# Optimization experiments

Measured on AMD Instinct MI355X. Metric: run time of the kernel, lower is better.

Reference implementation:

```python
import jax, jax.numpy as jnp
import numpy as np

N_NODES = 50000
N_EDGES = 800000
IN_CH, HID, OUT_CH, HEADS = 128, 32, 32, 8
NEG_SLOPE = 0.2


def setup_inputs() -> dict:
    key = jax.random.key(0)
    ks = jax.random.split(key, 20)
    x = jax.random.normal(ks[0], (N_NODES, IN_CH), dtype=jnp.float32)
    edge_index = jax.random.randint(ks[1], (2, N_EDGES), 0, N_NODES, dtype=jnp.int64)
    s = 0.1
    # encoder layer 1: in -> hid, heads=8 (concat)
    W1 = jax.random.normal(ks[2], (IN_CH, HEADS * HID), jnp.float32) * s
    as1 = jax.random.normal(ks[3], (HEADS, HID), jnp.float32) * s
    ad1 = jax.random.normal(ks[4], (HEADS, HID), jnp.float32) * s
    b1 = jnp.zeros((HEADS * HID,), jnp.float32)
    # encoder layer 2: hid*heads -> out, heads=1
    W2 = jax.random.normal(ks[5], (HEADS * HID, OUT_CH), jnp.float32) * s
    as2 = jax.random.normal(ks[6], (1, OUT_CH), jnp.float32) * s
    ad2 = jax.random.normal(ks[7], (1, OUT_CH), jnp.float32) * s
    b2 = jnp.zeros((OUT_CH,), jnp.float32)
    # decoder layer 1: out -> hid, heads=8 (concat)
    W3 = jax.random.normal(ks[8], (OUT_CH, HEADS * HID), jnp.float32) * s
    as3 = jax.random.normal(ks[9], (HEADS, HID), jnp.float32) * s
    ad3 = jax.random.normal(ks[10], (HEADS, HID), jnp.float32) * s
    b3 = jnp.zeros((HEADS * HID,), jnp.float32)
    # decoder layer 2: hid*heads -> in, heads=1
    W4 = jax.random.normal(ks[11], (HEADS * HID, IN_CH), jnp.float32) * s
    as4 = jax.random.normal(ks[12], (1, IN_CH), jnp.float32) * s
    ad4 = jax.random.normal(ks[13], (1, IN_CH), jnp.float32) * s
    b4 = jnp.zeros((IN_CH,), jnp.float32)
    return dict(x=x, edge_index=edge_index, W1=W1, as1=as1, ad1=ad1, b1=b1,
                W2=W2, as2=as2, ad2=ad2, b2=b2, W3=W3, as3=as3, ad3=ad3, b3=b3,
                W4=W4, as4=as4, ad4=ad4, b4=b4)


def gat_conv(x, src, dst, W, a_src, a_dst, b, heads, ch):
    # PyG GATConv: h = xW, e_ij = LeakyReLU(a_src.h_j + a_dst.h_i), softmax over incoming edges of i
    h = (x @ W).reshape(-1, heads, ch)                       # [N, H, C]
    al_s = jnp.sum(h * a_src[None], axis=-1)                 # [N, H]
    al_d = jnp.sum(h * a_dst[None], axis=-1)                 # [N, H]
    e = jax.nn.leaky_relu(al_s[src] + al_d[dst], NEG_SLOPE)  # [E, H]
    emax = jax.ops.segment_max(e, dst, num_segments=N_NODES)
    ee = jnp.exp(e - emax[dst])
    denom = jax.ops.segment_sum(ee, dst, num_segments=N_NODES)
    alpha = ee / denom[dst]                                  # [E, H]
    msg = alpha[:, :, None] * h[src]                         # [E, H, C]
    out = jax.ops.segment_sum(msg, dst, num_segments=N_NODES)  # [N, H, C]
    return out.reshape(N_NODES, heads * ch) + b


def reference(x, edge_index, W1, as1, ad1, b1, W2, as2, ad2, b2,
              W3, as3, ad3, b3, W4, as4, ad4, b4):
    # add self loops (PyG default add_self_loops=True)
    loop = jnp.arange(N_NODES, dtype=edge_index.dtype)
    src = jnp.concatenate([edge_index[0], loop])
    dst = jnp.concatenate([edge_index[1], loop])
    # encode
    z = gat_conv(x, src, dst, W1, as1, ad1, b1, HEADS, HID)
    z = jax.nn.relu(z)
    z = gat_conv(z, src, dst, W2, as2, ad2, b2, 1, OUT_CH)
    # decode
    r = gat_conv(z, src, dst, W3, as3, ad3, b3, HEADS, HID)
    r = jax.nn.relu(r)
    r = gat_conv(r, src, dst, W4, as4, ad4, b4, 1, IN_CH)
    return r
```

## Files before the change

kernel.cpp:

```cpp
#include <hip/hip_runtime.h>
#include <math.h>

#define N_NODES 50000
#define N_EDGES 800000
#define N_TOT   850000
#define NSB     ((N_NODES + 255) / 256)

typedef __attribute__((ext_vector_type(8))) short short8;
typedef __attribute__((ext_vector_type(4))) float floatx4;

__device__ __forceinline__ unsigned int pack_bf16x2(float a, float b) {
    unsigned ua = __float_as_uint(a);
    unsigned ub = __float_as_uint(b);
    ua += 0x7fff + ((ua >> 16) & 1);
    ub += 0x7fff + ((ub >> 16) & 1);
    return (ua >> 16) | (ub & 0xffff0000u);
}
__device__ __forceinline__ unsigned short pack_bf16(float a) {
    unsigned ua = __float_as_uint(a);
    ua += 0x7fff + ((ua >> 16) & 1);
    return (unsigned short)(ua >> 16);
}
__device__ __forceinline__ float bf16_lo(unsigned u) { return __uint_as_float(u << 16); }
__device__ __forceinline__ float bf16_hi(unsigned u) { return __uint_as_float(u & 0xffff0000u); }

__global__ void zero_int_kernel(int* p, int n) {
    int i = blockIdx.x * blockDim.x + threadIdx.x;
    if (i < n) p[i] = 0;
}

__global__ void deg_hist_kernel(const int* __restrict__ ei, int* __restrict__ deg) {
    int e = blockIdx.x * blockDim.x + threadIdx.x;
    if (e >= N_TOT) return;
    int dst = (e < N_EDGES) ? ei[N_EDGES + e] : (e - N_EDGES);
    atomicAdd(&deg[dst], 1);
}

__global__ void block_scan_kernel(const int* __restrict__ deg, int* __restrict__ part,
                                  int* __restrict__ bsum) {
    __shared__ int tmp[256];
    int t = threadIdx.x;
    int i = blockIdx.x * 256 + t;
    int v = (i < N_NODES) ? deg[i] : 0;
    tmp[t] = v;
    __syncthreads();
    for (int d = 1; d < 256; d <<= 1) {
        int u = (t >= d) ? tmp[t - d] : 0;
        __syncthreads();
        tmp[t] += u;
        __syncthreads();
    }
    if (i < N_NODES) part[i] = tmp[t] - v;
    if (t == 255) bsum[blockIdx.x] = tmp[255];
}

__global__ void scan_bsum_kernel(int* __restrict__ bsum) {
    __shared__ int tmp[256];
    int t = threadIdx.x;
    int v = (t < NSB) ? bsum[t] : 0;
    tmp[t] = v;
    __syncthreads();
    for (int d = 1; d < 256; d <<= 1) {
        int u = (t >= d) ? tmp[t - d] : 0;
        __syncthreads();
        tmp[t] += u;
        __syncthreads();
    }
    if (t < NSB) bsum[t] = tmp[t] - v;
}

__global__ void finalize_off_kernel(const int* __restrict__ part, const int* __restrict__ bsum,
                                    int* __restrict__ off, int* __restrict__ cursor) {
    int i = blockIdx.x * 256 + threadIdx.x;
    if (i < N_NODES) {
        int o = part[i] + bsum[blockIdx.x];
        off[i] = o;
        cursor[i] = o;
    }
    if (i == 0) off[N_NODES] = N_TOT;
}

__global__ void fill_csr_kernel(const int* __restrict__ ei, int* __restrict__ cursor,
                                int* __restrict__ csr_src) {
    int e = blockIdx.x * blockDim.x + threadIdx.x;
    if (e >= N_TOT) return;
    int src, dst;
    if (e < N_EDGES) { src = ei[e]; dst = ei[N_EDGES + e]; }
    else             { src = dst = e - N_EDGES; }
    int pos = atomicAdd(&cursor[dst], 1);
    csr_src[pos] = src;
}

__global__ void wconv_kernel(const float* __restrict__ W1, const float* __restrict__ W2,
                             const float* __restrict__ W3, const float* __restrict__ W4,
                             unsigned short* __restrict__ T1, unsigned short* __restrict__ T2,
                             unsigned short* __restrict__ T3, unsigned short* __restrict__ T4) {
    int i = blockIdx.x * 256 + threadIdx.x;
    const float* W; unsigned short* T; int K, N, idx;
    if      (i < 32768) { W = W1; T = T1; K = 128; N = 256; idx = i; }
    else if (i < 40960) { W = W2; T = T2; K = 256; N = 32;  idx = i - 32768; }
    else if (i < 49152) { W = W3; T = T3; K = 32;  N = 256; idx = i - 40960; }
    else if (i < 81920) { W = W4; T = T4; K = 256; N = 128; idx = i - 49152; }
    else return;
    int n = idx / K, k = idx % K;
    T[idx] = pack_bf16(W[(size_t)k * N + n]);
}

template<int Cin, int Cout, int H, int C, int NPB, int NW_N, bool IN_BF16>
__global__ void gemm_mfma_kernel(const void* __restrict__ xin,
                                 const unsigned short* __restrict__ Wt,
                                 const float* __restrict__ a_src, const float* __restrict__ a_dst,
                                 unsigned short* __restrict__ hb,
                                 float* __restrict__ al_s, float* __restrict__ al_d) {
    constexpr int NW_M = 4 / NW_N;
    constexpr int MT_W = (NPB / 16) / NW_M;
    constexpr int NT_W = (Cout / 16) / NW_N;
    constexpr int AS   = Cin + 8;
    constexpr int SP   = Cout + 4;
    __shared__ unsigned short xs[NPB * AS];
    __shared__ float hs[NPB * SP];
    int tid = threadIdx.x;
    int n0  = blockIdx.x * NPB;

    if (IN_BF16) {
        for (int i = tid; i < NPB * Cin / 8; i += 256) {
            int n = i / (Cin / 8), k8 = i % (Cin / 8);
            uint4 q = make_uint4(0u, 0u, 0u, 0u);
            if (n0 + n < N_NODES)
                q = ((const uint4*)((const unsigned short*)xin + (size_t)(n0 + n) * Cin))[k8];
            *(uint4*)(xs + n * AS + k8 * 8) = q;
        }
    } else {
        for (int i = tid; i < NPB * Cin / 4; i += 256) {
            int n = i / (Cin / 4), k4 = i % (Cin / 4);
            float4 v = make_float4(0.f, 0.f, 0.f, 0.f);
            if (n0 + n < N_NODES)
                v = ((const float4*)((const float*)xin + (size_t)(n0 + n) * Cin))[k4];
            uint2 p;
            p.x = pack_bf16x2(v.x, v.y);
            p.y = pack_bf16x2(v.z, v.w);
            *(uint2*)(xs + n * AS + k4 * 4) = p;
        }
    }
    __syncthreads();

    int w = tid >> 6, lane = tid & 63;
    int q = lane >> 4, l16 = lane & 15;
    int wm = w / NW_N, wn = w % NW_N;
    int mbase = wm * MT_W * 16;
    int nbase = wn * NT_W * 16;

    floatx4 acc[MT_W][NT_W];
#pragma unroll
    for (int mt = 0; mt < MT_W; mt++)
#pragma unroll
        for (int nt = 0; nt < NT_W; nt++) acc[mt][nt] = (floatx4){0.f, 0.f, 0.f, 0.f};

#pragma unroll
    for (int k0 = 0; k0 < Cin; k0 += 32) {
        short8 a[MT_W], b[NT_W];
#pragma unroll
        for (int mt = 0; mt < MT_W; mt++)
            a[mt] = *(const short8*)(xs + (mbase + mt * 16 + l16) * AS + k0 + q * 8);
#pragma unroll
        for (int nt = 0; nt < NT_W; nt++)
            b[nt] = *(const short8*)(Wt + (size_t)(nbase + nt * 16 + l16) * Cin + k0 + q * 8);
#pragma unroll
        for (int mt = 0; mt < MT_W; mt++)
#pragma unroll
            for (int nt = 0; nt < NT_W; nt++)
                acc[mt][nt] = __builtin_amdgcn_mfma_f32_16x16x32_bf16(a[mt], b[nt], acc[mt][nt], 0, 0, 0);
    }

#pragma unroll
    for (int mt = 0; mt < MT_W; mt++)
#pragma unroll
        for (int nt = 0; nt < NT_W; nt++)
#pragma unroll
            for (int r = 0; r < 4; r++) {
                int nl = mbase + mt * 16 + q * 4 + r;
                int ch = nbase + nt * 16 + l16;
                hs[nl * SP + ch] = acc[mt][nt][r];
            }
    __syncthreads();

    constexpr int TPN = Cout / 32;
    constexpr int TPH = (C > 32) ? (C / 32) : 1;
    if (tid < NPB * TPN) {
        int node = tid / TPN, sub = tid % TPN;
        int gn = n0 + node;
        int head = (sub * 32) / C;
        int coff = (sub * 32) % C;
        const float* hrow = hs + node * SP + sub * 32;
        const float* ap = a_src + head * C + coff;
        const float* dp = a_dst + head * C + coff;
        float ps = 0.f, pd = 0.f;
        unsigned pk[8];
#pragma unroll
        for (int c4 = 0; c4 < 8; c4++) {
            float4 hv = *(const float4*)(hrow + c4 * 4);
            float4 av = *(const float4*)(ap + c4 * 4);
            float4 dv = *(const float4*)(dp + c4 * 4);
            ps += hv.x * av.x + hv.y * av.y + hv.z * av.z + hv.w * av.w;
            pd += hv.x * dv.x + hv.y * dv.y + hv.z * dv.z + hv.w * dv.w;
            pk[c4] = pack_bf16x2(hv.x, hv.y) | 0u;
            pk[c4] = pack_bf16x2(hv.x, hv.y);
        }
        uint4 o0, o1;
        {
            float4 h0 = *(const float4*)(hrow + 0);
            float4 h1 = *(const float4*)(hrow + 4);
            float4 h2 = *(const float4*)(hrow + 8);
            float4 h3 = *(const float4*)(hrow + 12);
            o0.x = pack_bf16x2(h0.x, h0.y); o0.y = pack_bf16x2(h0.z, h0.w);
            o0.z = pack_bf16x2(h1.x, h1.y); o0.w = pack_bf16x2(h1.z, h1.w);
            o1.x = pack_bf16x2(h2.x, h2.y); o1.y = pack_bf16x2(h2.z, h2.w);
            o1.z = pack_bf16x2(h3.x, h3.y); o1.w = pack_bf16x2(h3.z, h3.w);
        }
        uint4 o2, o3;
        {
            float4 h0 = *(const float4*)(hrow + 16);
            float4 h1 = *(const float4*)(hrow + 20);
            float4 h2 = *(const float4*)(hrow + 24);
            float4 h3 = *(const float4*)(hrow + 28);
            o2.x = pack_bf16x2(h0.x, h0.y); o2.y = pack_bf16x2(h0.z, h0.w);
            o2.z = pack_bf16x2(h1.x, h1.y); o2.w = pack_bf16x2(h1.z, h1.w);
            o3.x = pack_bf16x2(h2.x, h2.y); o3.y = pack_bf16x2(h2.z, h2.w);
            o3.z = pack_bf16x2(h3.x, h3.y); o3.w = pack_bf16x2(h3.z, h3.w);
        }
        if (gn < N_NODES) {
            uint2* dst = (uint2*)(hb + (size_t)gn * Cout + sub * 32);
            dst[0] = make_uint2(o0.x, o0.y); dst[1] = make_uint2(o0.z, o0.w);
            dst[2] = make_uint2(o1.x, o1.y); dst[3] = make_uint2(o1.z, o1.w);
            dst[4] = make_uint2(o2.x, o2.y); dst[5] = make_uint2(o2.z, o2.w);
            dst[6] = make_uint2(o3.x, o3.y); dst[7] = make_uint2(o3.z, o3.w);
        }
        if (TPH > 1) {
#pragma unroll
            for (int k = 1; k < TPH; k <<= 1) {
                ps += __shfl_xor(ps, k, 64);
                pd += __shfl_xor(pd, k, 64);
            }
            if ((sub % TPH) == 0 && gn < N_NODES) {
                al_s[gn * H + head] = ps;
                al_d[gn * H + head] = pd;
            }
        } else {
            if (gn < N_NODES) {
                al_s[gn * H + head] = ps;
                al_d[gn * H + head] = pd;
            }
        }
    }
}

template<int H, int C, bool RELU, bool OUT_BF16>
__launch_bounds__(256, 8)
__global__ void gat_agg_kernel(const unsigned short* __restrict__ hb,
                               const float* __restrict__ al_s,
                               const float* __restrict__ al_d, const int* __restrict__ off,
                               const int* __restrict__ csr_src, const float* __restrict__ bias,
                               void* __restrict__ out) {
    constexpr int HC  = H * C;
    constexpr int G   = HC / 4;
    constexpr int SUB = G / H;
    constexpr int NPW = 64 / G;
    constexpr int NPB = 4 * NPW;

    int tid  = threadIdx.x;
    int wid  = tid >> 6;
    int lane = tid & 63;
    int gi   = lane / G;
    int g    = lane % G;
    int node = blockIdx.x * NPB + wid * NPW + gi;
    if (node >= N_NODES) return;

    int head = g / SUB;
    int es   = g % SUB;
    int r0 = off[node], r1 = off[node + 1];
    float ald = al_d[node * H + head];

    float m = -INFINITY, s = 0.f;
    for (int j = r0 + es; j < r1; j += SUB) {
        int src = csr_src[j];
        float e = al_s[src * H + head] + ald;
        e = (e > 0.f) ? e : 0.2f * e;
        float M = fmaxf(m, e);
        s = s * __expf(m - M) + __expf(e - M);
        m = M;
    }
#pragma unroll
    for (int k = 1; k < SUB; k <<= 1) {
        float om = __shfl_xor(m, k, 64);
        float os = __shfl_xor(s, k, 64);
        float M = fmaxf(m, om);
        float S;
        if (M == -INFINITY) S = 0.f;
        else S = s * __expf(m - M) + os * __expf(om - M);
        m = M; s = S;
    }
    float inv_s = 1.f / s;

    const uint2* hb2 = (const uint2*)hb;
    float4 acc = ((const float4*)bias)[g];
    int j0 = r0;
    for (; j0 + 8 <= r1; j0 += 8) {
        int srcs[8];
#pragma unroll
        for (int u = 0; u < 8; u++) srcs[u] = csr_src[j0 + u];
#pragma unroll
        for (int u = 0; u < 8; u++) {
            float e = al_s[srcs[u] * H + head] + ald;
            e = (e > 0.f) ? e : 0.2f * e;
            float we = __expf(e - m) * inv_s;
            uint2 q = hb2[(size_t)srcs[u] * (HC / 4) + g];
            acc.x += we * bf16_lo(q.x); acc.y += we * bf16_hi(q.x);
            acc.z += we * bf16_lo(q.y); acc.w += we * bf16_hi(q.y);
        }
    }
    for (; j0 < r1; j0++) {
        int src = csr_src[j0];
        float e = al_s[src * H + head] + ald;
        e = (e > 0.f) ? e : 0.2f * e;
        float we = __expf(e - m) * inv_s;
        uint2 q = hb2[(size_t)src * (HC / 4) + g];
        acc.x += we * bf16_lo(q.x); acc.y += we * bf16_hi(q.x);
        acc.z += we * bf16_lo(q.y); acc.w += we * bf16_hi(q.y);
    }
    if (RELU) {
        acc.x = fmaxf(acc.x, 0.f); acc.y = fmaxf(acc.y, 0.f);
        acc.z = fmaxf(acc.z, 0.f); acc.w = fmaxf(acc.w, 0.f);
    }
    if (OUT_BF16) {
        uint2 p;
        p.x = pack_bf16x2(acc.x, acc.y);
        p.y = pack_bf16x2(acc.z, acc.w);
        ((uint2*)out)[(size_t)node * (HC / 4) + g] = p;
    } else {
        ((float4*)out)[(size_t)node * (HC / 4) + g] = acc;
    }
}

extern "C" void kernel_launch(void* const* d_in, const int* in_sizes, int n_in,
                              void* d_out, int out_size, void* d_ws, size_t ws_size,
                              hipStream_t stream) {
    const float* x   = (const float*)d_in[0];
    const int*   ei  = (const int*)d_in[1];
    const float* W1  = (const float*)d_in[2];
    const float* as1 = (const float*)d_in[3];
    const float* ad1 = (const float*)d_in[4];
    const float* b1  = (const float*)d_in[5];
    const float* W2  = (const float*)d_in[6];
    const float* as2 = (const float*)d_in[7];
    const float* ad2 = (const float*)d_in[8];
    const float* b2  = (const float*)d_in[9];
    const float* W3  = (const float*)d_in[10];
    const float* as3 = (const float*)d_in[11];
    const float* ad3 = (const float*)d_in[12];
    const float* b3  = (const float*)d_in[13];
    const float* W4  = (const float*)d_in[14];
    const float* as4 = (const float*)d_in[15];
    const float* ad4 = (const float*)d_in[16];
    const float* b4  = (const float*)d_in[17];

    char* ws = (char*)d_ws;
    size_t o = 0;
    auto alloc = [&](size_t bytes) -> void* {
        void* p = ws + o;
        o = (o + bytes + 255) & ~(size_t)255;
        return p;
    };
    unsigned short* feat_a  = (unsigned short*)alloc((size_t)N_NODES * 256 * 2);
    unsigned short* feat_b  = (unsigned short*)alloc((size_t)N_NODES * 32 * 2);
    unsigned short* h_buf   = (unsigned short*)alloc((size_t)N_NODES * 256 * 2);
    float*          al_s    = (float*)alloc((size_t)N_NODES * 8 * 4);
    float*          al_d    = (float*)alloc((size_t)N_NODES * 8 * 4);
    int*            deg     = (int*)alloc((size_t)(N_NODES + 1) * 4);
    int*            off     = (int*)alloc((size_t)(N_NODES + 1) * 4);
    int*            cursor  = (int*)alloc((size_t)N_NODES * 4);
    int*            part    = (int*)alloc((size_t)N_NODES * 4);
    int*            bsum    = (int*)alloc((size_t)256 * 4);
    int*            csr_src = (int*)alloc((size_t)N_TOT * 4);
    unsigned short* w1t     = (unsigned short*)alloc(32768 * 2);
    unsigned short* w2t     = (unsigned short*)alloc(8192 * 2);
    unsigned short* w3t     = (unsigned short*)alloc(8192 * 2);
    unsigned short* w4t     = (unsigned short*)alloc(32768 * 2);

    const int TPB = 256;
    int nb_nodes = (N_NODES + TPB - 1) / TPB;
    int nb_edges = (N_TOT + TPB - 1) / TPB;

    zero_int_kernel<<<nb_nodes, TPB, 0, stream>>>(deg, N_NODES);
    wconv_kernel<<<320, TPB, 0, stream>>>(W1, W2, W3, W4, w1t, w2t, w3t, w4t);
    deg_hist_kernel<<<nb_edges, TPB, 0, stream>>>(ei, deg);
    block_scan_kernel<<<NSB, TPB, 0, stream>>>(deg, part, bsum);
    scan_bsum_kernel<<<1, TPB, 0, stream>>>(bsum);
    finalize_off_kernel<<<NSB, TPB, 0, stream>>>(part, bsum, off, cursor);
    fill_csr_kernel<<<nb_edges, TPB, 0, stream>>>(ei, cursor, csr_src);

    auto agg_blocks = [](int hc) { return (N_NODES * (hc / 4) + 255) / 256; };

    gemm_mfma_kernel<128, 256, 8, 32, 32, 4, false>
        <<<(N_NODES + 31) / 32, TPB, 0, stream>>>(x, w1t, as1, ad1, h_buf, al_s, al_d);
    gat_agg_kernel<8, 32, true, true><<<agg_blocks(256), TPB, 0, stream>>>(h_buf, al_s, al_d, off, csr_src, b1, feat_a);

    gemm_mfma_kernel<256, 32, 1, 32, 64, 2, true>
        <<<(N_NODES + 63) / 64, TPB, 0, stream>>>(feat_a, w2t, as2, ad2, h_buf, al_s, al_d);
    gat_agg_kernel<1, 32, false, true><<<agg_blocks(32), TPB, 0, stream>>>(h_buf, al_s, al_d, off, csr_src, b2, feat_b);

    gemm_mfma_kernel<32, 256, 8, 32, 32, 4, true>
        <<<(N_NODES + 31) / 32, TPB, 0, stream>>>(feat_b, w3t, as3, ad3, h_buf, al_s, al_d);
    gat_agg_kernel<8, 32, true, true><<<agg_blocks(256), TPB, 0, stream>>>(h_buf, al_s, al_d, off, csr_src, b3, feat_a);

    gemm_mfma_kernel<256, 128, 1, 128, 32, 4, true>
        <<<(N_NODES + 31) / 32, TPB, 0, stream>>>(feat_a, w4t, as4, ad4, h_buf, al_s, al_d);
    gat_agg_kernel<1, 128, false, false><<<agg_blocks(128), TPB, 0, stream>>>(h_buf, al_s, al_d, off, csr_src, b4, d_out);
}
```

Measured before the change: 546.6 us.

## Single-pass GAT aggregation with unnormalized exp weights shared via lane shuffles

```diff
diff --git a/kernel.cpp b/kernel.cpp
--- a/kernel.cpp
+++ b/kernel.cpp
@@ -195,7 +195,6 @@
         const float* ap = a_src + head * C + coff;
         const float* dp = a_dst + head * C + coff;
         float ps = 0.f, pd = 0.f;
-        unsigned pk[8];
 #pragma unroll
         for (int c4 = 0; c4 < 8; c4++) {
             float4 hv = *(const float4*)(hrow + c4 * 4);
@@ -203,8 +202,6 @@
             float4 dv = *(const float4*)(dp + c4 * 4);
             ps += hv.x * av.x + hv.y * av.y + hv.z * av.z + hv.w * av.w;
             pd += hv.x * dv.x + hv.y * dv.y + hv.z * dv.z + hv.w * dv.w;
-            pk[c4] = pack_bf16x2(hv.x, hv.y) | 0u;
-            pk[c4] = pack_bf16x2(hv.x, hv.y);
         }
         uint4 o0, o1;
         {
@@ -255,7 +252,7 @@
 }
 
 template<int H, int C, bool RELU, bool OUT_BF16>
-__launch_bounds__(256, 8)
+__launch_bounds__(256, 6)
 __global__ void gat_agg_kernel(const unsigned short* __restrict__ hb,
                                const float* __restrict__ al_s,
                                const float* __restrict__ al_d, const int* __restrict__ off,
@@ -266,6 +263,7 @@
     constexpr int SUB = G / H;
     constexpr int NPW = 64 / G;
     constexpr int NPB = 4 * NPW;
+    constexpr int UNR = (SUB > 8) ? 8 : SUB;
 
     int tid  = threadIdx.x;
     int wid  = tid >> 6;
@@ -277,56 +275,65 @@
 
     int head = g / SUB;
     int es   = g % SUB;
+    int nb   = lane & ~(G - 1);
     int r0 = off[node], r1 = off[node + 1];
     float ald = al_d[node * H + head];
 
-    float m = -INFINITY, s = 0.f;
-    for (int j = r0 + es; j < r1; j += SUB) {
-        int src = csr_src[j];
-        float e = al_s[src * H + head] + ald;
-        e = (e > 0.f) ? e : 0.2f * e;
-        float M = fmaxf(m, e);
-        s = s * __expf(m - M) + __expf(e - M);
-        m = M;
-    }
-#pragma unroll
-    for (int k = 1; k < SUB; k <<= 1) {
-        float om = __shfl_xor(m, k, 64);
-        float os = __shfl_xor(s, k, 64);
-        float M = fmaxf(m, om);
-        float S;
-        if (M == -INFINITY) S = 0.f;
-        else S = s * __expf(m - M) + os * __expf(om - M);
-        m = M; s = S;
-    }
-    float inv_s = 1.f / s;
-
     const uint2* hb2 = (const uint2*)hb;
-    float4 acc = ((const float4*)bias)[g];
+    float4 acc = make_float4(0.f, 0.f, 0.f, 0.f);
+    float wsum = 0.f;
+
     int j0 = r0;
-    for (; j0 + 8 <= r1; j0 += 8) {
-        int srcs[8];
-#pragma unroll
-        for (int u = 0; u < 8; u++) srcs[u] = csr_src[j0 + u];
-#pragma unroll
-        for (int u = 0; u < 8; u++) {
-            float e = al_s[srcs[u] * H + head] + ald;
-            e = (e > 0.f) ? e : 0.2f * e;
-            float we = __expf(e - m) * inv_s;
-            uint2 q = hb2[(size_t)srcs[u] * (HC / 4) + g];
-            acc.x += we * bf16_lo(q.x); acc.y += we * bf16_hi(q.x);
-            acc.z += we * bf16_lo(q.y); acc.w += we * bf16_hi(q.y);
-        }
-    }
-    for (; j0 < r1; j0++) {
-        int src = csr_src[j0];
-        float e = al_s[src * H + head] + ald;
-        e = (e > 0.f) ? e : 0.2f * e;
-        float we = __expf(e - m) * inv_s;
-        uint2 q = hb2[(size_t)src * (HC / 4) + g];
-        acc.x += we * bf16_lo(q.x); acc.y += we * bf16_hi(q.x);
-        acc.z += we * bf16_lo(q.y); acc.w += we * bf16_hi(q.y);
-    }
+    for (; j0 + SUB <= r1; j0 += SUB) {
+        int srcv = csr_src[j0 + es];
+        float e = al_s[srcv * H + head] + ald;
+        e = fmaxf(e, 0.2f * e);
+        float wv = __expf(e);
+        for (int u0 = 0; u0 < SUB; u0 += UNR) {
+#pragma unroll
+            for (int uu = 0; uu < UNR; uu++) {
+                int u = u0 + uu;
+                float wu = __shfl(wv, nb + head * SUB + u, 64);
+                int su;
+                if (NPW == 1) su = __builtin_amdgcn_readlane(srcv, u);
+                else          su = __shfl(srcv, nb + u, 64);
+                uint2 qv = hb2[(size_t)su * G + g];
+                wsum  += wu;
+                acc.x += wu * bf16_lo(qv.x); acc.y += wu * bf16_hi(qv.x);
+                acc.z += wu * bf16_lo(qv.y); acc.w += wu * bf16_hi(qv.y);
+            }
+        }
+    }
+    if (j0 < r1) {
+        bool valid = (j0 + es) < r1;
+        int srcv = csr_src[valid ? (j0 + es) : (r1 - 1)];
+        float e = al_s[srcv * H + head] + ald;
+        e = fmaxf(e, 0.2f * e);
+        float wv = valid ? __expf(e) : 0.f;
+        for (int u0 = 0; u0 < SUB; u0 += UNR) {
+#pragma unroll
+            for (int uu = 0; uu < UNR; uu++) {
+                int u = u0 + uu;
+                float wu = __shfl(wv, nb + head * SUB + u, 64);
+                if (wu != 0.f) {
+                    int su;
+                    if (NPW == 1) su = __builtin_amdgcn_readlane(srcv, u);
+                    else          su = __shfl(srcv, nb + u, 64);
+                    uint2 qv = hb2[(size_t)su * G + g];
+                    wsum  += wu;
+                    acc.x += wu * bf16_lo(qv.x); acc.y += wu * bf16_hi(qv.x);
+                    acc.z += wu * bf16_lo(qv.y); acc.w += wu * bf16_hi(qv.y);
+                }
+            }
+        }
+    }
+
+    float inv = 1.f / wsum;
+    float4 bv = ((const float4*)bias)[g];
+    acc.x = acc.x * inv + bv.x;
+    acc.y = acc.y * inv + bv.y;
+    acc.z = acc.z * inv + bv.z;
+    acc.w = acc.w * inv + bv.w;
     if (RELU) {
         acc.x = fmaxf(acc.x, 0.f); acc.y = fmaxf(acc.y, 0.f);
         acc.z = fmaxf(acc.z, 0.f); acc.w = fmaxf(acc.w, 0.f);
```

New measurement: 500.6 us. -8.4%, faster.
